# Performance work log

Measured on AMD Instinct MI355X. Metric: run time of the kernel, lower is better.

Reference implementation:

```python
import jax, jax.numpy as jnp
import numpy as np

B, L, D_MODEL = 4, 2048, 2048
N_HEADS, HEAD_DIM = 16, 128
EPS = 1e-6


def _make_rope(key_unused, L, dim, base=10000.0):
    inv_freq = 1.0 / (base ** (np.arange(0, dim, 2, dtype=np.float32) / dim))  # [dim/2]
    t = np.arange(L, dtype=np.float32)
    freqs = np.outer(t, inv_freq)  # [L, dim/2]
    emb = np.concatenate([freqs, freqs], axis=-1)  # [L, dim]
    cos = np.broadcast_to(np.cos(emb)[None], (B, L, dim)).copy()
    sin = np.broadcast_to(np.sin(emb)[None], (B, L, dim)).copy()
    return jnp.asarray(cos), jnp.asarray(sin)


def setup_inputs() -> dict:
    key = jax.random.key(0)
    ks = jax.random.split(key, 8)
    s = 1.0 / np.sqrt(D_MODEL)
    x = jax.random.normal(ks[0], (B, L, D_MODEL), dtype=jnp.float32)
    cos_q, sin_q = _make_rope(None, L, HEAD_DIM)
    cos_k, sin_k = _make_rope(None, L, HEAD_DIM)
    Wq = jax.random.normal(ks[1], (D_MODEL, D_MODEL), dtype=jnp.float32) * s
    Wk = jax.random.normal(ks[2], (D_MODEL, D_MODEL), dtype=jnp.float32) * s
    Wv = jax.random.normal(ks[3], (D_MODEL, D_MODEL), dtype=jnp.float32) * s
    Wo = jax.random.normal(ks[4], (D_MODEL, D_MODEL), dtype=jnp.float32) * s
    q_gamma = jnp.ones((HEAD_DIM,), dtype=jnp.float32) + 0.02 * jax.random.normal(ks[5], (HEAD_DIM,), dtype=jnp.float32)
    k_gamma = jnp.ones((HEAD_DIM,), dtype=jnp.float32) + 0.02 * jax.random.normal(ks[6], (HEAD_DIM,), dtype=jnp.float32)
    return dict(x=x, cos_q=cos_q, sin_q=sin_q, cos_k=cos_k, sin_k=sin_k,
                Wq=Wq, Wk=Wk, Wv=Wv, Wo=Wo, q_gamma=q_gamma, k_gamma=k_gamma)


def _rms_norm(h, w):
    # T5-style RMSNorm over last dim (head_dim), variance in fp32
    var = jnp.mean(h.astype(jnp.float32) ** 2, axis=-1, keepdims=True)
    return w * (h * jax.lax.rsqrt(var + EPS))


def _rotate_half(x):
    d = x.shape[-1] // 2
    return jnp.concatenate([-x[..., d:], x[..., :d]], axis=-1)


def _apply_rope(x, cos, sin):
    # x: [B, L, H, Dh]; cos/sin: [B, L, Dh] -> broadcast over heads
    c = cos[:, :, None, :]
    s = sin[:, :, None, :]
    return x * c + _rotate_half(x) * s


def reference(x, cos_q, sin_q, cos_k, sin_k, Wq, Wk, Wv, Wo, q_gamma, k_gamma):
    Bx, Lx, _ = x.shape
    # QKV projections (Linear with weight [out, in]: y = x @ W.T)
    q = (x @ Wq.T).reshape(Bx, Lx, N_HEADS, HEAD_DIM)
    k = (x @ Wk.T).reshape(Bx, Lx, N_HEADS, HEAD_DIM)
    v = (x @ Wv.T).reshape(Bx, Lx, N_HEADS, HEAD_DIM)
    # per-head QK RMSNorm
    q = _rms_norm(q, q_gamma)
    k = _rms_norm(k, k_gamma)
    # dual RoPE
    q = _apply_rope(q, cos_q, sin_q)
    k = _apply_rope(k, cos_k, sin_k)
    # scaled dot-product attention (dense, no mask)
    scale = 1.0 / jnp.sqrt(jnp.asarray(HEAD_DIM, dtype=x.dtype))
    scores = jnp.einsum('blhd,bmhd->bhlm', q, k) * scale
    attn = jax.nn.softmax(scores, axis=-1)
    out = jnp.einsum('bhlm,bmhd->blhd', attn, v)
    out = out.reshape(Bx, Lx, N_HEADS * HEAD_DIM)
    return out @ Wo.T
```

## Files before the change

### kernel.cpp

```cpp
#include <hip/hip_runtime.h>
#include <stdint.h>

#define DM   2048
#define LSEQ 2048
#define NB   4
#define NH   16
#define HD   128
#define BL   (NB*LSEQ)

typedef unsigned short u16;
typedef short  short8 __attribute__((ext_vector_type(8)));
typedef float  f32x4  __attribute__((ext_vector_type(4)));
typedef float  f32x16 __attribute__((ext_vector_type(16)));

#define LOG2E 1.4426950408889634f

__device__ __forceinline__ float bf2f(u16 v) {
    union { unsigned u; float f; } x; x.u = ((unsigned)v) << 16; return x.f;
}
__device__ __forceinline__ u16 f2bf(float f) {
    union { float f; unsigned u; } x; x.f = f;
    return (u16)((x.u + 0x7FFF + ((x.u >> 16) & 1)) >> 16);
}

__device__ __forceinline__ short8 ld8(const void* base, size_t e, bool f32) {
    if (f32) {
        const float* p = (const float*)base + e;
        f32x4 a = *(const f32x4*)p;
        f32x4 b = *(const f32x4*)(p + 4);
        short8 r;
        #pragma unroll
        for (int i = 0; i < 4; ++i) { r[i] = (short)f2bf(a[i]); r[4+i] = (short)f2bf(b[i]); }
        return r;
    }
    return *(const short8*)((const u16*)base + e);
}
__device__ __forceinline__ float lde(const void* b, size_t e, bool f32) {
    return f32 ? ((const float*)b)[e] : bf2f(((const u16*)b)[e]);
}
__device__ __forceinline__ void st1(void* b, size_t e, float v, bool f32) {
    if (f32) ((float*)b)[e] = v; else ((u16*)b)[e] = f2bf(v);
}

extern "C" __global__ void dtype_probe(const u16* __restrict__ x, int* __restrict__ cnt) {
    int t = threadIdx.x;
    int insane = 0;
    #pragma unroll
    for (int j = 0; j < 16; ++j) {
        u16 u = x[t * 16 + j];
        int e = (u >> 7) & 0xFF;
        if (u != 0 && (e < 96 || e > 143)) insane++;
    }
    atomicAdd(cnt, insane);
}

extern "C" __global__ void to_bf16(const void* __restrict__ in, u16* __restrict__ out,
                                   int n8, const int* __restrict__ cnt)
{
    const bool isf = *cnt > 100;
    int i = blockIdx.x * 256 + threadIdx.x;
    if (i >= n8) return;
    *(short8*)(out + (size_t)i * 8) = ld8(in, (size_t)i * 8, isf);
}

extern "C" __global__ void to_bf16_w(const void* w0, const void* w1,
                                     const void* w2, const void* w3,
                                     u16* o0, u16* o1, u16* o2, u16* o3,
                                     int n8, const int* __restrict__ cnt)
{
    const bool isf = *cnt > 100;
    int i = blockIdx.x * 256 + threadIdx.x;
    if (i >= n8) return;
    const void* in; u16* out;
    switch (blockIdx.y) {
        case 0:  in = w0; out = o0; break;
        case 1:  in = w1; out = o1; break;
        case 2:  in = w2; out = o2; break;
        default: in = w3; out = o3; break;
    }
    *(short8*)(out + (size_t)i * 8) = ld8(in, (size_t)i * 8, isf);
}

__device__ __forceinline__ int swz128(int row, int col) {
    return row*128 + ((((col >> 3) ^ row) & 15) << 3) + (col & 7);
}
__device__ __forceinline__ int swz64(int row, int col) {
    return row*64 + ((((col >> 3) ^ row) & 7) << 3) + (col & 7);
}

__device__ __forceinline__ void xcd_swz(int& bx, int& by, int& bz) {
    const int lin = blockIdx.x + (blockIdx.y << 4) + (blockIdx.z << 10);
    const int nq  = (gridDim.z << 10) >> 3;
    const int nid = (lin & 7) * nq + (lin >> 3);
    bx = nid & 15; by = (nid >> 4) & 63; bz = nid >> 10;
}

typedef __attribute__((address_space(1))) const unsigned int guint;
typedef __attribute__((address_space(3))) unsigned int luint;
__device__ __forceinline__ void gl_lds16(const void* g, void* l) {
    __builtin_amdgcn_global_load_lds((guint*)g, (luint*)l, 16, 0, 0);
}

__device__ __forceinline__ void gemm_core_bf(const u16* __restrict__ A,
                                             const u16* __restrict__ W,
                                             u16* Al, u16* Bl,
                                             f32x4 acc[4][4],
                                             int m0, int n0, int t)
{
    const int lane = t & 63, w = t >> 6;
    const int quad = lane >> 4, l15 = lane & 15;
    const int wm = (w >> 1) * 64, wn = (w & 1) * 64;
    const int srow = w * 16 + (lane >> 2);
    const int scol = (lane & 3) * 8;
    const u16* ag = A + (size_t)(m0 + srow) * DM + scol;
    const u16* wg = W + (size_t)(n0 + srow) * DM + scol;
    u16* al0 = Al + (w * 16) * 32;
    u16* al1 = Al + (64 + w * 16) * 32;
    u16* bl0 = Bl + (w * 16) * 32;
    u16* bl1 = Bl + (64 + w * 16) * 32;

    for (int k0 = 0; k0 < DM; k0 += 32) {
        __syncthreads();
        gl_lds16(ag + k0,                   al0);
        gl_lds16(ag + k0 + (size_t)64 * DM, al1);
        gl_lds16(wg + k0,                   bl0);
        gl_lds16(wg + k0 + (size_t)64 * DM, bl1);
        __syncthreads();
        short8 afr[4], bfr[4];
        #pragma unroll
        for (int mt = 0; mt < 4; ++mt)
            afr[mt] = *(const short8*)&Al[(wm + mt*16 + l15)*32 + quad*8];
        #pragma unroll
        for (int nt = 0; nt < 4; ++nt)
            bfr[nt] = *(const short8*)&Bl[(wn + nt*16 + l15)*32 + quad*8];
        #pragma unroll
        for (int mt = 0; mt < 4; ++mt)
            #pragma unroll
            for (int nt = 0; nt < 4; ++nt)
                acc[mt][nt] = __builtin_amdgcn_mfma_f32_16x16x32_bf16(
                                  afr[mt], bfr[nt], acc[mt][nt], 0, 0, 0);
    }
}

extern "C" __global__ __launch_bounds__(256) void gemm_bf(
    const u16* __restrict__ A, const u16* __restrict__ W,
    void* __restrict__ O, const int* __restrict__ cnt, int o_sel)
{
    __shared__ __align__(16) u16 Al[128*32];
    __shared__ __align__(16) u16 Bl[128*32];
    const bool of = o_sel && (*cnt > 100);
    int bx, by, bz;  xcd_swz(bx, by, bz);
    const int n0 = bx * 128, m0 = by * 128;
    const int t = threadIdx.x, lane = t & 63, w = t >> 6;
    const int quad = lane >> 4, l15 = lane & 15;
    const int wm = (w >> 1) * 64, wn = (w & 1) * 64;

    f32x4 acc[4][4];
    #pragma unroll
    for (int i = 0; i < 4; ++i)
        #pragma unroll
        for (int j = 0; j < 4; ++j) acc[i][j] = (f32x4){0.f, 0.f, 0.f, 0.f};

    gemm_core_bf(A, W, Al, Bl, acc, m0, n0, t);

    #pragma unroll
    for (int mt = 0; mt < 4; ++mt)
        #pragma unroll
        for (int r = 0; r < 4; ++r) {
            size_t base = (size_t)(m0 + wm + mt*16 + quad*4 + r) * DM + n0 + wn + l15;
            #pragma unroll
            for (int nt = 0; nt < 4; ++nt) st1(O, base + nt*16, acc[mt][nt][r], of);
        }
}

extern "C" __global__ __launch_bounds__(256) void gemm_qk2(
    const u16* __restrict__ A, const u16* __restrict__ W0, const u16* __restrict__ W1,
    u16* __restrict__ O0, u16* __restrict__ O1)
{
    __shared__ __align__(16) u16 Al[128*32];
    __shared__ __align__(16) u16 Bl[128*32];
    int bx, by, bz;  xcd_swz(bx, by, bz);
    const u16* W = bz ? W1 : W0;
    u16*       O = bz ? O1 : O0;
    const int n0 = bx * 128, m0 = by * 128;
    const int t = threadIdx.x, lane = t & 63, w = t >> 6;
    const int quad = lane >> 4, l15 = lane & 15;
    const int wm = (w >> 1) * 64, wn = (w & 1) * 64;

    f32x4 acc[4][4];
    #pragma unroll
    for (int i = 0; i < 4; ++i)
        #pragma unroll
        for (int j = 0; j < 4; ++j) acc[i][j] = (f32x4){0.f, 0.f, 0.f, 0.f};

    gemm_core_bf(A, W, Al, Bl, acc, m0, n0, t);

    #pragma unroll
    for (int mt = 0; mt < 4; ++mt)
        #pragma unroll
        for (int r = 0; r < 4; ++r) {
            size_t base = (size_t)(m0 + wm + mt*16 + quad*4 + r) * DM + n0 + wn + l15;
            #pragma unroll
            for (int nt = 0; nt < 4; ++nt) O[base + nt*16] = f2bf(acc[mt][nt][r]);
        }
}

extern "C" __global__ __launch_bounds__(256) void gemm_vb(
    const u16* __restrict__ A, const u16* __restrict__ W, u16* __restrict__ vT)
{
    __shared__ __align__(16) u16 Al[128*32];
    __shared__ __align__(16) u16 Bl[128*32];
    __shared__ __align__(16) u16 Tl[128*128];
    int bx, by, bz;  xcd_swz(bx, by, bz);
    const int n0 = bx * 128, m0 = by * 128;
    const int t = threadIdx.x, lane = t & 63, w = t >> 6;
    const int quad = lane >> 4, l15 = lane & 15;
    const int wm = (w >> 1) * 64, wn = (w & 1) * 64;

    f32x4 acc[4][4];
    #pragma unroll
    for (int i = 0; i < 4; ++i)
        #pragma unroll
        for (int j = 0; j < 4; ++j) acc[i][j] = (f32x4){0.f, 0.f, 0.f, 0.f};

    gemm_core_bf(A, W, Al, Bl, acc, m0, n0, t);

    #pragma unroll
    for (int mt = 0; mt < 4; ++mt)
        #pragma unroll
        for (int nt = 0; nt < 4; ++nt)
            #pragma unroll
            for (int r = 0; r < 4; ++r) {
                int m = wm + mt*16 + quad*4 + r;
                int n = wn + nt*16 + l15;
                Tl[swz128(n, m)] = f2bf(acc[mt][nt][r]);
            }
    __syncthreads();
    const int b  = m0 >> 11;
    const int l0 = m0 & (LSEQ - 1);
    #pragma unroll
    for (int it = 0; it < 8; ++it) {
        int c = t + 256*it;
        int nr = c >> 4, m8 = (c & 15) * 8;
        short8 val = *(const short8*)&Tl[swz128(nr, m8)];
        *(short8*)(vT + (size_t)b*DM*LSEQ + (size_t)(n0 + nr)*LSEQ + l0 + m8) = val;
    }
}

extern "C" __global__ void rmsrope(u16* __restrict__ q, u16* __restrict__ kk,
    const void* cq, const void* sq, const void* ck, const void* sk,
    const void* qg, const void* kg, const int* cnt)
{
    const bool isf = *cnt > 100;
    const float slc = 0.08838834764831845f * LOG2E;
    int t = blockIdx.x * 256 + threadIdx.x;
    int lane = t & 63;
    int widx = t >> 6;
    int h  = widx & (NH - 1);
    int bl = widx >> 4;
    size_t ro = (size_t)bl * DM + (size_t)h * HD;
    size_t co = (size_t)bl * HD;

    {
        float e0 = bf2f(q[ro + lane]), e1 = bf2f(q[ro + lane + 64]);
        float ss = e0*e0 + e1*e1;
        #pragma unroll
        for (int sm = 1; sm < 64; sm <<= 1) ss += __shfl_xor(ss, sm, 64);
        float r = rsqrtf(ss * (1.f / HD) + 1e-6f);
        float y0 = e0 * r * lde(qg, lane, isf);
        float y1 = e1 * r * lde(qg, lane + 64, isf);
        float c0 = lde(cq, co + lane, isf), c1 = lde(cq, co + lane + 64, isf);
        float s0 = lde(sq, co + lane, isf), s1 = lde(sq, co + lane + 64, isf);
        q[ro + lane]      = f2bf((y0 * c0 - y1 * s0) * slc);
        q[ro + lane + 64] = f2bf((y1 * c1 + y0 * s1) * slc);
    }
    {
        float e0 = bf2f(kk[ro + lane]), e1 = bf2f(kk[ro + lane + 64]);
        float ss = e0*e0 + e1*e1;
        #pragma unroll
        for (int sm = 1; sm < 64; sm <<= 1) ss += __shfl_xor(ss, sm, 64);
        float r = rsqrtf(ss * (1.f / HD) + 1e-6f);
        float y0 = e0 * r * lde(kg, lane, isf);
        float y1 = e1 * r * lde(kg, lane + 64, isf);
        float c0 = lde(ck, co + lane, isf), c1 = lde(ck, co + lane + 64, isf);
        float s0 = lde(sk, co + lane, isf), s1 = lde(sk, co + lane + 64, isf);
        kk[ro + lane]      = f2bf(y0 * c0 - y1 * s0);
        kk[ro + lane + 64] = f2bf(y1 * c1 + y0 * s1);
    }
}

extern "C" __global__ __launch_bounds__(256, 2) void flash(
    const u16* q, const u16* __restrict__ k,
    const u16* __restrict__ vT, u16* o)
{
    __shared__ __align__(16) u16 lds[32768];

    const int bh = blockIdx.x, b = bh >> 4, h = bh & 15;
    const int q0 = blockIdx.y * 128;
    const int t = threadIdx.x, lane = t & 63, w = t >> 6;
    const int l31 = lane & 31, hi8 = (lane >> 5) * 8;
    const size_t qko = (size_t)b * LSEQ * DM + (size_t)h * HD;
    const size_t vo  = (size_t)b * DM * LSEQ + (size_t)h * HD * LSEQ;

    short8 qf[8];
    #pragma unroll
    for (int ks = 0; ks < 8; ++ks)
        qf[ks] = *(const short8*)(q + qko +
                  (size_t)(q0 + w*32 + l31) * DM + ks*16 + hi8);

    f32x16 zz;
    #pragma unroll
    for (int r = 0; r < 16; ++r) zz[r] = 0.f;
    f32x16 acc[4];
    f32x16 dacc;
    #pragma unroll
    for (int dt = 0; dt < 4; ++dt) acc[dt] = zz;
    dacc = zz;

    const short onev = (l31 == 0) ? (short)0x3F80 : (short)0;
    const short8 onesA = {onev, onev, onev, onev, onev, onev, onev, onev};

    const int krow = t >> 4,  kc8 = (t & 15) * 8;
    const int vrow = t >> 3,  vc8 = (t & 7) * 8;
    short8 kreg[4], vreg[4];

    #pragma unroll
    for (int it = 0; it < 4; ++it) {
        kreg[it] = *(const short8*)(k  + qko + (size_t)(krow + it*16) * DM + kc8);
        vreg[it] = *(const short8*)(vT + vo  + (size_t)(vrow + it*32) * LSEQ + vc8);
    }
    {
        u16* Kn = lds;  u16* Vn = lds + 8192;
        #pragma unroll
        for (int it = 0; it < 4; ++it) {
            *(short8*)&Kn[swz128(krow + it*16, kc8)] = kreg[it];
            *(short8*)&Vn[swz64 (vrow + it*32, vc8)] = vreg[it];
        }
    }
    #pragma unroll
    for (int it = 0; it < 4; ++it) {
        kreg[it] = *(const short8*)(k  + qko + (size_t)(64 + krow + it*16) * DM + kc8);
        vreg[it] = *(const short8*)(vT + vo  + (size_t)(vrow + it*32) * LSEQ + 64 + vc8);
    }
    __syncthreads();

    const int NT = LSEQ / 64;
    for (int it0 = 0; it0 < NT; ++it0) {
        const int cur = it0 & 1;
        if (it0 + 1 < NT) {
            u16* Kn = lds + (cur ^ 1) * 16384;
            u16* Vn = Kn + 8192;
            #pragma unroll
            for (int it = 0; it < 4; ++it) {
                *(short8*)&Kn[swz128(krow + it*16, kc8)] = kreg[it];
                *(short8*)&Vn[swz64 (vrow + it*32, vc8)] = vreg[it];
            }
        }
        if (it0 + 2 < NT) {
            const int kv = (it0 + 2) * 64;
            #pragma unroll
            for (int it = 0; it < 4; ++it) {
                kreg[it] = *(const short8*)(k  + qko + (size_t)(kv + krow + it*16) * DM + kc8);
                vreg[it] = *(const short8*)(vT + vo  + (size_t)(vrow + it*32) * LSEQ + kv + vc8);
            }
        }
        u16* Kl = lds + cur * 16384;
        u16* Vl = Kl + 8192;

        f32x16 S0, S1;
        __builtin_amdgcn_s_setprio(1);
        {
            short8 kf0 = *(const short8*)&Kl[swz128(l31,      hi8)];
            short8 kf1 = *(const short8*)&Kl[swz128(32 + l31, hi8)];
            S0 = __builtin_amdgcn_mfma_f32_32x32x16_bf16(kf0, qf[0], zz, 0, 0, 0);
            S1 = __builtin_amdgcn_mfma_f32_32x32x16_bf16(kf1, qf[0], zz, 0, 0, 0);
        }
        #pragma unroll
        for (int ks = 1; ks < 8; ++ks) {
            short8 kf0 = *(const short8*)&Kl[swz128(l31,      ks*16 + hi8)];
            short8 kf1 = *(const short8*)&Kl[swz128(32 + l31, ks*16 + hi8)];
            S0 = __builtin_amdgcn_mfma_f32_32x32x16_bf16(kf0, qf[ks], S0, 0, 0, 0);
            S1 = __builtin_amdgcn_mfma_f32_32x32x16_bf16(kf1, qf[ks], S1, 0, 0, 0);
        }
        __builtin_amdgcn_s_setprio(0);

        float p[32];
        #pragma unroll
        for (int r = 0; r < 16; ++r) p[r]      = exp2f(S0[r]);
        #pragma unroll
        for (int r = 0; r < 16; ++r) p[16 + r] = exp2f(S1[r]);

        #pragma unroll
        for (int kt = 0; kt < 2; ++kt) {
            unsigned pk[8];
            #pragma unroll
            for (int j = 0; j < 8; ++j)
                asm("v_cvt_pk_bf16_f32 %0, %1, %2"
                    : "=v"(pk[j]) : "v"(p[kt*16 + 2*j]), "v"(p[kt*16 + 2*j + 1]));
            asm volatile("v_permlane32_swap_b32 %0, %1" : "+v"(pk[0]), "+v"(pk[2]));
            asm volatile("v_permlane32_swap_b32 %0, %1" : "+v"(pk[1]), "+v"(pk[3]));
            asm volatile("v_permlane32_swap_b32 %0, %1" : "+v"(pk[4]), "+v"(pk[6]));
            asm volatile("v_permlane32_swap_b32 %0, %1" : "+v"(pk[5]), "+v"(pk[7]));
            union { unsigned u[4]; short8 v; } f0, f1;
            f0.u[0] = pk[0]; f0.u[1] = pk[1]; f0.u[2] = pk[2]; f0.u[3] = pk[3];
            f1.u[0] = pk[4]; f1.u[1] = pk[5]; f1.u[2] = pk[6]; f1.u[3] = pk[7];
            #pragma unroll
            for (int s = 0; s < 2; ++s) {
                short8 pf = s ? f1.v : f0.v;
                int slice = kt*2 + s;
                __builtin_amdgcn_s_setprio(1);
                #pragma unroll
                for (int dt = 0; dt < 4; ++dt) {
                    short8 vf = *(const short8*)&Vl[swz64(dt*32 + l31, slice*16 + hi8)];
                    acc[dt] = __builtin_amdgcn_mfma_f32_32x32x16_bf16(vf, pf, acc[dt], 0, 0, 0);
                }
                dacc = __builtin_amdgcn_mfma_f32_32x32x16_bf16(onesA, pf, dacc, 0, 0, 0);
                __builtin_amdgcn_s_setprio(0);
            }
        }
        __syncthreads();
    }

    u16* Ol = lds + w * 4352;
    float dn0 = dacc[0];
    float dnx = __shfl_xor(dn0, 32, 64);
    float inv = 1.f / ((lane & 32) ? dnx : dn0);
    #pragma unroll
    for (int dt = 0; dt < 4; ++dt)
        #pragma unroll
        for (int i = 0; i < 8; ++i) {
            float a0 = acc[dt][2*i]     * inv;
            float a1 = acc[dt][2*i + 1] * inv;
            unsigned pkv;
            asm("v_cvt_pk_bf16_f32 %0, %1, %2" : "=v"(pkv) : "v"(a0), "v"(a1));
            int d = dt*32 + ((i & 1) << 1) + ((i >> 1) << 3) + ((lane >> 5) << 2);
            *(unsigned*)&Ol[l31*136 + d] = pkv;
        }
    __syncthreads();
    #pragma unroll
    for (int j = 0; j < 8; ++j) {
        int cb = (lane >> 5) + 2*j;
        short8 vv = *(const short8*)&Ol[l31*136 + cb*8];
        *(short8*)(o + qko + (size_t)(q0 + w*32 + l31) * DM + cb*8) = vv;
    }
}

extern "C" void kernel_launch(void* const* d_in, const int* in_sizes, int n_in,
                              void* d_out, int out_size, void* d_ws, size_t ws_size,
                              hipStream_t stream)
{
    const void* x  = d_in[0];
    const void* cq = d_in[1];
    const void* sq = d_in[2];
    const void* ck = d_in[3];
    const void* sk = d_in[4];
    const void* Wq = d_in[5];
    const void* Wk = d_in[6];
    const void* Wv = d_in[7];
    const void* Wo = d_in[8];
    const void* qg = d_in[9];
    const void* kg = d_in[10];

    u16* qws = (u16*)d_ws;
    u16* kws = qws + (size_t)BL * DM;
    u16* vtw = kws + (size_t)BL * DM;
    u16* wqs = vtw + (size_t)BL * DM;
    u16* wks = wqs + (size_t)DM * DM;
    u16* wvs = wks + (size_t)DM * DM;
    u16* wos = wvs + (size_t)DM * DM;
    int* cnt = (int*)(wos + (size_t)DM * DM);
    u16* xb  = (u16*)d_out;

    const int xn8 = BL * DM / 8;
    const int wn8 = DM * DM / 8;

    hipMemsetAsync(cnt, 0, 4, stream);
    dtype_probe<<<1, 256, 0, stream>>>((const u16*)x, cnt);

    to_bf16<<<xn8 / 256, 256, 0, stream>>>(x, xb, xn8, cnt);
    to_bf16_w<<<dim3(wn8 / 256, 4), 256, 0, stream>>>(Wq, Wk, Wv, Wo,
                                                      wqs, wks, wvs, wos, wn8, cnt);

    gemm_vb <<<dim3(16, 64),    256, 0, stream>>>(xb, wvs, vtw);
    gemm_qk2<<<dim3(16, 64, 2), 256, 0, stream>>>(xb, wqs, wks, qws, kws);

    rmsrope<<<dim3(BL * NH / 4), 256, 0, stream>>>(qws, kws, cq, sq, ck, sk, qg, kg, cnt);

    flash<<<dim3(64, 16), 256, 0, stream>>>(qws, kws, vtw, qws);

    gemm_bf<<<dim3(16, 64), 256, 0, stream>>>(qws, wos, d_out, cnt, 1);
}
```

Before: 752.1 us.

## Use 256x256 GEMM tiles with triple-buffered async LDS pipeline

```diff
diff --git a/kernel.cpp b/kernel.cpp
--- a/kernel.cpp
+++ b/kernel.cpp
@@ -7,11 +7,13 @@
 #define NH   16
 #define HD   128
 #define BL   (NB*LSEQ)
+#define NK64 (DM/32)
 
 typedef unsigned short u16;
-typedef short  short8 __attribute__((ext_vector_type(8)));
-typedef float  f32x4  __attribute__((ext_vector_type(4)));
-typedef float  f32x16 __attribute__((ext_vector_type(16)));
+typedef short  short8  __attribute__((ext_vector_type(8)));
+typedef short  short4v __attribute__((ext_vector_type(4)));
+typedef float  f32x4   __attribute__((ext_vector_type(4)));
+typedef float  f32x16  __attribute__((ext_vector_type(16)));
 
 #define LOG2E 1.4426950408889634f
 
@@ -88,11 +90,11 @@
     return row*64 + ((((col >> 3) ^ row) & 7) << 3) + (col & 7);
 }
 
-__device__ __forceinline__ void xcd_swz(int& bx, int& by, int& bz) {
-    const int lin = blockIdx.x + (blockIdx.y << 4) + (blockIdx.z << 10);
-    const int nq  = (gridDim.z << 10) >> 3;
+__device__ __forceinline__ void xcd_swz8(int& bx, int& by, int& bz) {
+    const int lin = blockIdx.x + (blockIdx.y << 3) + (blockIdx.z << 8);
+    const int nq  = (gridDim.z << 8) >> 3;
     const int nid = (lin & 7) * nq + (lin >> 3);
-    bx = nid & 15; by = (nid >> 4) & 63; bz = nid >> 10;
+    bx = nid & 7; by = (nid >> 3) & 31; bz = nid >> 8;
 }
 
 typedef __attribute__((address_space(1))) const unsigned int guint;
@@ -101,150 +103,147 @@
     __builtin_amdgcn_global_load_lds((guint*)g, (luint*)l, 16, 0, 0);
 }
 
-__device__ __forceinline__ void gemm_core_bf(const u16* __restrict__ A,
-                                             const u16* __restrict__ W,
-                                             u16* Al, u16* Bl,
-                                             f32x4 acc[4][4],
-                                             int m0, int n0, int t)
+__device__ __forceinline__ void g256_stage(const u16* ag, const u16* wg,
+                                           u16* buf, int k0, int wofs)
+{
+    gl_lds16(ag + k0,                    buf + wofs);
+    gl_lds16(ag + k0 + (size_t)128 * DM, buf + 4096 + wofs);
+    gl_lds16(wg + k0,                    buf + 8192 + wofs);
+    gl_lds16(wg + k0 + (size_t)128 * DM, buf + 12288 + wofs);
+}
+
+__device__ __forceinline__ void g256_core(const u16* __restrict__ A,
+                                          const u16* __restrict__ W,
+                                          u16* lds, f32x4 acc[8][4],
+                                          int m0, int n0, int t)
 {
     const int lane = t & 63, w = t >> 6;
     const int quad = lane >> 4, l15 = lane & 15;
-    const int wm = (w >> 1) * 64, wn = (w & 1) * 64;
-    const int srow = w * 16 + (lane >> 2);
-    const int scol = (lane & 3) * 8;
+    const int wr = (w >> 2) * 128, wc = (w & 3) * 64;
+    const int srow = t >> 2, scol = (t & 3) * 8;
     const u16* ag = A + (size_t)(m0 + srow) * DM + scol;
     const u16* wg = W + (size_t)(n0 + srow) * DM + scol;
-    u16* al0 = Al + (w * 16) * 32;
-    u16* al1 = Al + (64 + w * 16) * 32;
-    u16* bl0 = Bl + (w * 16) * 32;
-    u16* bl1 = Bl + (64 + w * 16) * 32;
-
-    for (int k0 = 0; k0 < DM; k0 += 32) {
-        __syncthreads();
-        gl_lds16(ag + k0,                   al0);
-        gl_lds16(ag + k0 + (size_t)64 * DM, al1);
-        gl_lds16(wg + k0,                   bl0);
-        gl_lds16(wg + k0 + (size_t)64 * DM, bl1);
-        __syncthreads();
-        short8 afr[4], bfr[4];
-        #pragma unroll
-        for (int mt = 0; mt < 4; ++mt)
-            afr[mt] = *(const short8*)&Al[(wm + mt*16 + l15)*32 + quad*8];
+    const int wofs = w * 512;
+
+    #pragma unroll
+    for (int i = 0; i < 8; ++i)
+        #pragma unroll
+        for (int j = 0; j < 4; ++j) acc[i][j] = (f32x4){0.f, 0.f, 0.f, 0.f};
+
+    g256_stage(ag, wg, lds,          0, wofs);
+    g256_stage(ag, wg, lds + 16384, 32, wofs);
+    asm volatile("s_waitcnt vmcnt(4)" ::: "memory");
+    __builtin_amdgcn_sched_barrier(0);
+    __builtin_amdgcn_s_barrier();
+    __builtin_amdgcn_sched_barrier(0);
+
+    int cur = 0, nx2 = 2;
+    for (int kt = 0; kt < NK64; ++kt) {
+        if (kt + 2 < NK64)
+            g256_stage(ag, wg, lds + nx2 * 16384, (kt + 2) * 32, wofs);
+        const u16* Ab = lds + cur * 16384;
+        const u16* Bb = Ab + 8192;
+        short8 afr[8], bfr[4];
         #pragma unroll
         for (int nt = 0; nt < 4; ++nt)
-            bfr[nt] = *(const short8*)&Bl[(wn + nt*16 + l15)*32 + quad*8];
-        #pragma unroll
-        for (int mt = 0; mt < 4; ++mt)
+            bfr[nt] = *(const short8*)&Bb[(wc + nt*16 + l15)*32 + quad*8];
+        #pragma unroll
+        for (int mt = 0; mt < 8; ++mt)
+            afr[mt] = *(const short8*)&Ab[(wr + mt*16 + l15)*32 + quad*8];
+        __builtin_amdgcn_s_setprio(1);
+        #pragma unroll
+        for (int mt = 0; mt < 8; ++mt)
             #pragma unroll
             for (int nt = 0; nt < 4; ++nt)
                 acc[mt][nt] = __builtin_amdgcn_mfma_f32_16x16x32_bf16(
                                   afr[mt], bfr[nt], acc[mt][nt], 0, 0, 0);
-    }
-}
-
-extern "C" __global__ __launch_bounds__(256) void gemm_bf(
+        __builtin_amdgcn_s_setprio(0);
+        if (kt + 2 < NK64) asm volatile("s_waitcnt vmcnt(4)" ::: "memory");
+        else               asm volatile("s_waitcnt vmcnt(0)" ::: "memory");
+        __builtin_amdgcn_sched_barrier(0);
+        __builtin_amdgcn_s_barrier();
+        __builtin_amdgcn_sched_barrier(0);
+        cur = (cur == 2) ? 0 : cur + 1;
+        nx2 = (nx2 == 2) ? 0 : nx2 + 1;
+    }
+}
+
+extern "C" __global__ __launch_bounds__(512, 2) void gemm256_bf(
     const u16* __restrict__ A, const u16* __restrict__ W,
     void* __restrict__ O, const int* __restrict__ cnt, int o_sel)
 {
-    __shared__ __align__(16) u16 Al[128*32];
-    __shared__ __align__(16) u16 Bl[128*32];
+    __shared__ __align__(16) u16 lds[49152];
     const bool of = o_sel && (*cnt > 100);
-    int bx, by, bz;  xcd_swz(bx, by, bz);
-    const int n0 = bx * 128, m0 = by * 128;
-    const int t = threadIdx.x, lane = t & 63, w = t >> 6;
+    int bx, by, bz;  xcd_swz8(bx, by, bz);
+    const int n0 = bx * 256, m0 = by * 256;
+    const int t = threadIdx.x, lane = t & 63;
     const int quad = lane >> 4, l15 = lane & 15;
-    const int wm = (w >> 1) * 64, wn = (w & 1) * 64;
-
-    f32x4 acc[4][4];
-    #pragma unroll
-    for (int i = 0; i < 4; ++i)
-        #pragma unroll
-        for (int j = 0; j < 4; ++j) acc[i][j] = (f32x4){0.f, 0.f, 0.f, 0.f};
-
-    gemm_core_bf(A, W, Al, Bl, acc, m0, n0, t);
-
-    #pragma unroll
-    for (int mt = 0; mt < 4; ++mt)
+    const int wr = ((t >> 6) >> 2) * 128, wc = ((t >> 6) & 3) * 64;
+
+    f32x4 acc[8][4];
+    g256_core(A, W, lds, acc, m0, n0, t);
+
+    #pragma unroll
+    for (int mt = 0; mt < 8; ++mt)
         #pragma unroll
         for (int r = 0; r < 4; ++r) {
-            size_t base = (size_t)(m0 + wm + mt*16 + quad*4 + r) * DM + n0 + wn + l15;
+            size_t base = (size_t)(m0 + wr + mt*16 + quad*4 + r) * DM + n0 + wc + l15;
             #pragma unroll
             for (int nt = 0; nt < 4; ++nt) st1(O, base + nt*16, acc[mt][nt][r], of);
         }
 }
 
-extern "C" __global__ __launch_bounds__(256) void gemm_qk2(
+extern "C" __global__ __launch_bounds__(512, 2) void gemm256_qk2(
     const u16* __restrict__ A, const u16* __restrict__ W0, const u16* __restrict__ W1,
     u16* __restrict__ O0, u16* __restrict__ O1)
 {
-    __shared__ __align__(16) u16 Al[128*32];
-    __shared__ __align__(16) u16 Bl[128*32];
-    int bx, by, bz;  xcd_swz(bx, by, bz);
+    __shared__ __align__(16) u16 lds[49152];
+    int bx, by, bz;  xcd_swz8(bx, by, bz);
     const u16* W = bz ? W1 : W0;
     u16*       O = bz ? O1 : O0;
-    const int n0 = bx * 128, m0 = by * 128;
-    const int t = threadIdx.x, lane = t & 63, w = t >> 6;
+    const int n0 = bx * 256, m0 = by * 256;
+    const int t = threadIdx.x, lane = t & 63;
     const int quad = lane >> 4, l15 = lane & 15;
-    const int wm = (w >> 1) * 64, wn = (w & 1) * 64;
-
-    f32x4 acc[4][4];
-    #pragma unroll
-    for (int i = 0; i < 4; ++i)
-        #pragma unroll
-        for (int j = 0; j < 4; ++j) acc[i][j] = (f32x4){0.f, 0.f, 0.f, 0.f};
-
-    gemm_core_bf(A, W, Al, Bl, acc, m0, n0, t);
-
-    #pragma unroll
-    for (int mt = 0; mt < 4; ++mt)
+    const int wr = ((t >> 6) >> 2) * 128, wc = ((t >> 6) & 3) * 64;
+
+    f32x4 acc[8][4];
+    g256_core(A, W, lds, acc, m0, n0, t);
+
+    #pragma unroll
+    for (int mt = 0; mt < 8; ++mt)
         #pragma unroll
         for (int r = 0; r < 4; ++r) {
-            size_t base = (size_t)(m0 + wm + mt*16 + quad*4 + r) * DM + n0 + wn + l15;
+            size_t base = (size_t)(m0 + wr + mt*16 + quad*4 + r) * DM + n0 + wc + l15;
             #pragma unroll
             for (int nt = 0; nt < 4; ++nt) O[base + nt*16] = f2bf(acc[mt][nt][r]);
         }
 }
 
-extern "C" __global__ __launch_bounds__(256) void gemm_vb(
+extern "C" __global__ __launch_bounds__(512, 2) void gemm256_vb(
     const u16* __restrict__ A, const u16* __restrict__ W, u16* __restrict__ vT)
 {
-    __shared__ __align__(16) u16 Al[128*32];
-    __shared__ __align__(16) u16 Bl[128*32];
-    __shared__ __align__(16) u16 Tl[128*128];
-    int bx, by, bz;  xcd_swz(bx, by, bz);
-    const int n0 = bx * 128, m0 = by * 128;
-    const int t = threadIdx.x, lane = t & 63, w = t >> 6;
+    __shared__ __align__(16) u16 lds[49152];
+    int bx, by, bz;  xcd_swz8(bx, by, bz);
+    const int n0 = bx * 256, m0 = by * 256;
+    const int t = threadIdx.x, lane = t & 63;
     const int quad = lane >> 4, l15 = lane & 15;
-    const int wm = (w >> 1) * 64, wn = (w & 1) * 64;
-
-    f32x4 acc[4][4];
-    #pragma unroll
-    for (int i = 0; i < 4; ++i)
-        #pragma unroll
-        for (int j = 0; j < 4; ++j) acc[i][j] = (f32x4){0.f, 0.f, 0.f, 0.f};
-
-    gemm_core_bf(A, W, Al, Bl, acc, m0, n0, t);
-
-    #pragma unroll
-    for (int mt = 0; mt < 4; ++mt)
-        #pragma unroll
-        for (int nt = 0; nt < 4; ++nt)
-            #pragma unroll
-            for (int r = 0; r < 4; ++r) {
-                int m = wm + mt*16 + quad*4 + r;
-                int n = wn + nt*16 + l15;
-                Tl[swz128(n, m)] = f2bf(acc[mt][nt][r]);
-            }
-    __syncthreads();
+    const int wr = ((t >> 6) >> 2) * 128, wc = ((t >> 6) & 3) * 64;
+
+    f32x4 acc[8][4];
+    g256_core(A, W, lds, acc, m0, n0, t);
+
     const int b  = m0 >> 11;
-    const int l0 = m0 & (LSEQ - 1);
-    #pragma unroll
-    for (int it = 0; it < 8; ++it) {
-        int c = t + 256*it;
-        int nr = c >> 4, m8 = (c & 15) * 8;
-        short8 val = *(const short8*)&Tl[swz128(nr, m8)];
-        *(short8*)(vT + (size_t)b*DM*LSEQ + (size_t)(n0 + nr)*LSEQ + l0 + m8) = val;
-    }
+    const int l0 = (m0 & (LSEQ - 1)) + wr + quad*4;
+    #pragma unroll
+    for (int mt = 0; mt < 8; ++mt)
+        #pragma unroll
+        for (int nt = 0; nt < 4; ++nt) {
+            short4v sv;
+            #pragma unroll
+            for (int r = 0; r < 4; ++r) sv[r] = (short)f2bf(acc[mt][nt][r]);
+            int n = n0 + wc + nt*16 + l15;
+            *(short4v*)(vT + (size_t)b*DM*LSEQ + (size_t)n*LSEQ + l0 + mt*16) = sv;
+        }
 }
 
 extern "C" __global__ void rmsrope(u16* __restrict__ q, u16* __restrict__ kk,
@@ -481,12 +480,12 @@
     to_bf16_w<<<dim3(wn8 / 256, 4), 256, 0, stream>>>(Wq, Wk, Wv, Wo,
                                                       wqs, wks, wvs, wos, wn8, cnt);
 
-    gemm_vb <<<dim3(16, 64),    256, 0, stream>>>(xb, wvs, vtw);
-    gemm_qk2<<<dim3(16, 64, 2), 256, 0, stream>>>(xb, wqs, wks, qws, kws);
+    gemm256_vb <<<dim3(8, 32),    512, 0, stream>>>(xb, wvs, vtw);
+    gemm256_qk2<<<dim3(8, 32, 2), 512, 0, stream>>>(xb, wqs, wks, qws, kws);
 
     rmsrope<<<dim3(BL * NH / 4), 256, 0, stream>>>(qws, kws, cq, sq, ck, sk, qg, kg, cnt);
 
     flash<<<dim3(64, 16), 256, 0, stream>>>(qws, kws, vtw, qws);
 
-    gemm_bf<<<dim3(16, 64), 256, 0, stream>>>(qws, wos, d_out, cnt, 1);
-}
+    gemm256_bf<<<dim3(8, 32), 512, 0, stream>>>(qws, wos, d_out, cnt, 1);
+}
```

After: 684.2 us. 9.0% less time.
